# Kernel optimization log

Measured on AMD Instinct MI355X. Metric: run time of the kernel, lower is better.

Reference implementation:

```python
import jax, jax.numpy as jnp
import numpy as np

HIDDEN = 1024
SENT = 1024
NS = 8192
NK = 8192


def setup_inputs() -> dict:
    key = jax.random.key(0)
    ks = jax.random.split(key, 6)
    scale = 0.02
    return {
        "sentences_embedding": jax.random.normal(ks[0], (NS, SENT), dtype=jnp.float32),
        "knowledge_embedding": jax.random.normal(ks[1], (NK, 2 * HIDDEN), dtype=jnp.float32),
        "Ws": jax.random.normal(ks[2], (HIDDEN, SENT), dtype=jnp.float32) * scale,
        "bs": jnp.zeros((HIDDEN,), dtype=jnp.float32),
        "Wk": jax.random.normal(ks[3], (HIDDEN, 2 * HIDDEN), dtype=jnp.float32) * scale,
        "bk": jnp.zeros((HIDDEN,), dtype=jnp.float32),
    }


def reference(sentences_embedding, knowledge_embedding, Ws, bs, Wk, bk):
    # S: [Ns, hidden], K: [Nk, hidden] (torch Linear: x @ W.T + b)
    S = sentences_embedding @ Ws.T + bs
    K = knowledge_embedding @ Wk.T + bk
    V = knowledge_embedding  # [Nk, 2*hidden]
    scores = S @ K.T  # [Ns, Nk]
    # NOTE: softmax over dim=0 (across sentences), per the original module
    attns = jax.nn.softmax(scores, axis=0)
    fused_knowledge = attns @ V  # [Ns, 2*hidden]
    return (attns, fused_knowledge)
```

## Files before the change

kernel.cpp:

```cpp
#include <hip/hip_runtime.h>
#include <hip/hip_bf16.h>
#include <math.h>

typedef __bf16 bf16_t;
typedef __bf16 bf16x8 __attribute__((ext_vector_type(8)));
typedef __bf16 bf16x4v __attribute__((ext_vector_type(4)));
typedef float floatx4 __attribute__((ext_vector_type(4)));

#define BM 128
#define BN 128
#define BK 64
#define LDT 72

__device__ __forceinline__ void gload_lds16(const void* g, void* l) {
    __builtin_amdgcn_global_load_lds(
        (__attribute__((address_space(1))) void*)g,
        (__attribute__((address_space(3))) void*)l,
        16, 0, 0);
}

__device__ __forceinline__ void split8(const float* p, bf16x8& hi, bf16x8& lo) {
    const float4* q = (const float4*)p;
    float4 a = q[0], b = q[1];
    float v[8] = { a.x, a.y, a.z, a.w, b.x, b.y, b.z, b.w };
#pragma unroll
    for (int i = 0; i < 8; ++i) {
        bf16_t h = (bf16_t)v[i];
        hi[i] = h;
        lo[i] = (bf16_t)(v[i] - (float)h);
    }
}

__device__ __forceinline__ bf16x8 ld8cvt(const float* p) {
    const float4* q = (const float4*)p;
    float4 a = q[0], b = q[1];
    bf16x8 r;
    r[0] = (bf16_t)a.x; r[1] = (bf16_t)a.y; r[2] = (bf16_t)a.z; r[3] = (bf16_t)a.w;
    r[4] = (bf16_t)b.x; r[5] = (bf16_t)b.y; r[6] = (bf16_t)b.z; r[7] = (bf16_t)b.w;
    return r;
}

template<bool OUT_SPLIT, bool HAS_BIAS>
__global__ __launch_bounds__(256, 2)
void gemm_nt_split(const float* __restrict__ A, const float* __restrict__ B,
                   const float* __restrict__ bias,
                   void* __restrict__ C0, bf16_t* __restrict__ Clo,
                   int M, int N, int K)
{
    __shared__ bf16_t Ah[BM * LDT];
    __shared__ bf16_t Al[BM * LDT];
    __shared__ bf16_t Bh[BN * LDT];
    __shared__ bf16_t Bl[BN * LDT];

    const int t    = threadIdx.x;
    const int m0   = blockIdx.x * BM;
    const int n0   = blockIdx.y * BN;
    const int lane = t & 63;
    const int wm   = ((t >> 6) & 1) * 64;
    const int wn   = (t >> 7) * 64;
    const int lr   = lane & 15;
    const int lg   = lane >> 4;

    floatx4 acc[4][4] = {};

    for (int k0 = 0; k0 < K; k0 += BK) {
#pragma unroll
        for (int i = 0; i < 4; ++i) {
            int idx = t + i * 256;
            int row = idx >> 3;
            int col = (idx & 7) << 3;
            bf16x8 h, l;
            split8(&A[(size_t)(m0 + row) * K + k0 + col], h, l);
            *(bf16x8*)&Ah[row * LDT + col] = h;
            *(bf16x8*)&Al[row * LDT + col] = l;
            split8(&B[(size_t)(n0 + row) * K + k0 + col], h, l);
            *(bf16x8*)&Bh[row * LDT + col] = h;
            *(bf16x8*)&Bl[row * LDT + col] = l;
        }
        __syncthreads();
#pragma unroll
        for (int ks = 0; ks < BK; ks += 32) {
            bf16x8 ah[4], al[4], bh[4], bl[4];
#pragma unroll
            for (int mi = 0; mi < 4; ++mi) {
                ah[mi] = *(const bf16x8*)&Ah[(wm + mi * 16 + lr) * LDT + ks + lg * 8];
                al[mi] = *(const bf16x8*)&Al[(wm + mi * 16 + lr) * LDT + ks + lg * 8];
            }
#pragma unroll
            for (int ni = 0; ni < 4; ++ni) {
                bh[ni] = *(const bf16x8*)&Bh[(wn + ni * 16 + lr) * LDT + ks + lg * 8];
                bl[ni] = *(const bf16x8*)&Bl[(wn + ni * 16 + lr) * LDT + ks + lg * 8];
            }
#pragma unroll
            for (int mi = 0; mi < 4; ++mi)
#pragma unroll
                for (int ni = 0; ni < 4; ++ni) {
                    acc[mi][ni] = __builtin_amdgcn_mfma_f32_16x16x32_bf16(ah[mi], bh[ni], acc[mi][ni], 0, 0, 0);
                    acc[mi][ni] = __builtin_amdgcn_mfma_f32_16x16x32_bf16(ah[mi], bl[ni], acc[mi][ni], 0, 0, 0);
                    acc[mi][ni] = __builtin_amdgcn_mfma_f32_16x16x32_bf16(al[mi], bh[ni], acc[mi][ni], 0, 0, 0);
                }
        }
        __syncthreads();
    }

#pragma unroll
    for (int mi = 0; mi < 4; ++mi)
#pragma unroll
        for (int ni = 0; ni < 4; ++ni) {
            int col = n0 + wn + ni * 16 + lr;
            float bv = 0.0f;
            if constexpr (HAS_BIAS) bv = bias[col];
#pragma unroll
            for (int r = 0; r < 4; ++r) {
                int row = m0 + wm + mi * 16 + lg * 4 + r;
                float v = acc[mi][ni][r] + bv;
                if constexpr (OUT_SPLIT) {
                    bf16_t h = (bf16_t)v;
                    ((bf16_t*)C0)[(size_t)row * N + col] = h;
                    Clo[(size_t)row * N + col] = (bf16_t)(v - (float)h);
                } else {
                    ((float*)C0)[(size_t)row * N + col] = v;
                }
            }
        }
}

__global__ __launch_bounds__(256, 2)
void gemm_nt_pre_async(const bf16_t* __restrict__ Ahi, const bf16_t* __restrict__ Alo,
                       const bf16_t* __restrict__ Bhi, const bf16_t* __restrict__ Blo,
                       float* __restrict__ C, int M, int N, int K)
{
    __shared__ bf16_t Ah[BM * BK];
    __shared__ bf16_t Al[BM * BK];
    __shared__ bf16_t Bh[BN * BK];
    __shared__ bf16_t Bl[BN * BK];

    const int t    = threadIdx.x;
    const int m0   = blockIdx.x * BM;
    const int n0   = blockIdx.y * BN;
    const int lane = t & 63;
    const int wv   = t >> 6;
    const int wm   = ((t >> 6) & 1) * 64;
    const int wn   = (t >> 7) * 64;
    const int lr   = lane & 15;
    const int lg   = lane >> 4;
    const int lrow = lane >> 3;
    const int lcol = (((lane & 7) ^ lrow) * 8);
    const int swz  = (lr & 7) << 3;

    floatx4 acc[4][4] = {};

    for (int k0 = 0; k0 < K; k0 += BK) {
#pragma unroll
        for (int i = 0; i < 4; ++i) {
            const int seg = wv * 4 + i;
            const int row = seg * 8 + lrow;
            const size_t ga = (size_t)(m0 + row) * K + k0 + lcol;
            const size_t gb = (size_t)(n0 + row) * K + k0 + lcol;
            gload_lds16(&Ahi[ga], &Ah[seg * 512]);
            gload_lds16(&Alo[ga], &Al[seg * 512]);
            gload_lds16(&Bhi[gb], &Bh[seg * 512]);
            gload_lds16(&Blo[gb], &Bl[seg * 512]);
        }
        __syncthreads();
#pragma unroll
        for (int ks = 0; ks < BK; ks += 32) {
            const int cA = (ks + lg * 8) ^ swz;
            bf16x8 ah[4], al[4], bh[4], bl[4];
#pragma unroll
            for (int mi = 0; mi < 4; ++mi) {
                ah[mi] = *(const bf16x8*)&Ah[(wm + mi * 16 + lr) * BK + cA];
                al[mi] = *(const bf16x8*)&Al[(wm + mi * 16 + lr) * BK + cA];
            }
#pragma unroll
            for (int ni = 0; ni < 4; ++ni) {
                bh[ni] = *(const bf16x8*)&Bh[(wn + ni * 16 + lr) * BK + cA];
                bl[ni] = *(const bf16x8*)&Bl[(wn + ni * 16 + lr) * BK + cA];
            }
#pragma unroll
            for (int mi = 0; mi < 4; ++mi)
#pragma unroll
                for (int ni = 0; ni < 4; ++ni) {
                    acc[mi][ni] = __builtin_amdgcn_mfma_f32_16x16x32_bf16(ah[mi], bh[ni], acc[mi][ni], 0, 0, 0);
                    acc[mi][ni] = __builtin_amdgcn_mfma_f32_16x16x32_bf16(ah[mi], bl[ni], acc[mi][ni], 0, 0, 0);
                    acc[mi][ni] = __builtin_amdgcn_mfma_f32_16x16x32_bf16(al[mi], bh[ni], acc[mi][ni], 0, 0, 0);
                }
        }
        __syncthreads();
    }

#pragma unroll
    for (int mi = 0; mi < 4; ++mi)
#pragma unroll
        for (int ni = 0; ni < 4; ++ni) {
            int col = n0 + wn + ni * 16 + lr;
#pragma unroll
            for (int r = 0; r < 4; ++r) {
                int row = m0 + wm + mi * 16 + lg * 4 + r;
                C[(size_t)row * N + col] = acc[mi][ni][r];
            }
        }
}

__global__ __launch_bounds__(256, 2)
void gemm_nt_bf16_async(const bf16_t* __restrict__ A, const bf16_t* __restrict__ B,
                        float* __restrict__ C, int M, int N, int K)
{
    __shared__ bf16_t As[BM * BK];
    __shared__ bf16_t Bs[BN * BK];

    const int t    = threadIdx.x;
    const int m0   = blockIdx.x * BM;
    const int n0   = blockIdx.y * BN;
    const int lane = t & 63;
    const int wv   = t >> 6;
    const int wm   = ((t >> 6) & 1) * 64;
    const int wn   = (t >> 7) * 64;
    const int lr   = lane & 15;
    const int lg   = lane >> 4;
    const int lrow = lane >> 3;
    const int lcol = (((lane & 7) ^ lrow) * 8);
    const int swz  = (lr & 7) << 3;

    floatx4 acc[4][4] = {};

    for (int k0 = 0; k0 < K; k0 += BK) {
#pragma unroll
        for (int i = 0; i < 4; ++i) {
            const int seg = wv * 4 + i;
            const int row = seg * 8 + lrow;
            gload_lds16(&A[(size_t)(m0 + row) * K + k0 + lcol], &As[seg * 512]);
            gload_lds16(&B[(size_t)(n0 + row) * K + k0 + lcol], &Bs[seg * 512]);
        }
        __syncthreads();
#pragma unroll
        for (int ks = 0; ks < BK; ks += 32) {
            const int cA = (ks + lg * 8) ^ swz;
            bf16x8 a[4], b[4];
#pragma unroll
            for (int mi = 0; mi < 4; ++mi)
                a[mi] = *(const bf16x8*)&As[(wm + mi * 16 + lr) * BK + cA];
#pragma unroll
            for (int ni = 0; ni < 4; ++ni)
                b[ni] = *(const bf16x8*)&Bs[(wn + ni * 16 + lr) * BK + cA];
#pragma unroll
            for (int mi = 0; mi < 4; ++mi)
#pragma unroll
                for (int ni = 0; ni < 4; ++ni)
                    acc[mi][ni] = __builtin_amdgcn_mfma_f32_16x16x32_bf16(
                        a[mi], b[ni], acc[mi][ni], 0, 0, 0);
        }
        __syncthreads();
    }

#pragma unroll
    for (int mi = 0; mi < 4; ++mi)
#pragma unroll
        for (int ni = 0; ni < 4; ++ni) {
            int col = n0 + wn + ni * 16 + lr;
#pragma unroll
            for (int r = 0; r < 4; ++r) {
                int row = m0 + wm + mi * 16 + lg * 4 + r;
                C[(size_t)row * N + col] = acc[mi][ni][r];
            }
        }
}

__global__ __launch_bounds__(256, 2)
void gemm_nn_f32(const float* __restrict__ A, const float* __restrict__ B,
                 float* __restrict__ C, int M, int N, int K)
{
    __shared__ bf16_t As[BM * LDT];
    __shared__ bf16_t Bs[BN * LDT];

    const int t    = threadIdx.x;
    const int m0   = blockIdx.x * BM;
    const int n0   = blockIdx.y * BN;
    const int lane = t & 63;
    const int wm   = ((t >> 6) & 1) * 64;
    const int wn   = (t >> 7) * 64;
    const int lr   = lane & 15;
    const int lg   = lane >> 4;

    floatx4 acc[4][4] = {};

    for (int k0 = 0; k0 < K; k0 += BK) {
#pragma unroll
        for (int i = 0; i < 4; ++i) {
            int idx = t + i * 256;
            int row = idx >> 3;
            int col = (idx & 7) << 3;
            *(bf16x8*)&As[row * LDT + col] = ld8cvt(&A[(size_t)(m0 + row) * K + k0 + col]);
        }
#pragma unroll
        for (int i = 0; i < 2; ++i) {
            int idx = t + i * 256;
            int pn  = (idx & 31) << 2;
            int pk  = (idx >> 5) << 2;
            const float* src = &B[(size_t)(k0 + pk) * N + n0 + pn];
            float4 r0 = *(const float4*)(src);
            float4 r1 = *(const float4*)(src + N);
            float4 r2 = *(const float4*)(src + 2 * (size_t)N);
            float4 r3 = *(const float4*)(src + 3 * (size_t)N);
            bf16x4v c0 = { (bf16_t)r0.x, (bf16_t)r1.x, (bf16_t)r2.x, (bf16_t)r3.x };
            bf16x4v c1 = { (bf16_t)r0.y, (bf16_t)r1.y, (bf16_t)r2.y, (bf16_t)r3.y };
            bf16x4v c2 = { (bf16_t)r0.z, (bf16_t)r1.z, (bf16_t)r2.z, (bf16_t)r3.z };
            bf16x4v c3 = { (bf16_t)r0.w, (bf16_t)r1.w, (bf16_t)r2.w, (bf16_t)r3.w };
            *(bf16x4v*)&Bs[(pn + 0) * LDT + pk] = c0;
            *(bf16x4v*)&Bs[(pn + 1) * LDT + pk] = c1;
            *(bf16x4v*)&Bs[(pn + 2) * LDT + pk] = c2;
            *(bf16x4v*)&Bs[(pn + 3) * LDT + pk] = c3;
        }
        __syncthreads();
#pragma unroll
        for (int ks = 0; ks < BK; ks += 32) {
            bf16x8 af[4], bfr[4];
#pragma unroll
            for (int mi = 0; mi < 4; ++mi)
                af[mi] = *(const bf16x8*)&As[(wm + mi * 16 + lr) * LDT + ks + lg * 8];
#pragma unroll
            for (int ni = 0; ni < 4; ++ni)
                bfr[ni] = *(const bf16x8*)&Bs[(wn + ni * 16 + lr) * LDT + ks + lg * 8];
#pragma unroll
            for (int mi = 0; mi < 4; ++mi)
#pragma unroll
                for (int ni = 0; ni < 4; ++ni)
                    acc[mi][ni] = __builtin_amdgcn_mfma_f32_16x16x32_bf16(
                        af[mi], bfr[ni], acc[mi][ni], 0, 0, 0);
        }
        __syncthreads();
    }

#pragma unroll
    for (int mi = 0; mi < 4; ++mi)
#pragma unroll
        for (int ni = 0; ni < 4; ++ni) {
            int col = n0 + wn + ni * 16 + lr;
#pragma unroll
            for (int r = 0; r < 4; ++r) {
                int row = m0 + wm + mi * 16 + lg * 4 + r;
                C[(size_t)row * N + col] = acc[mi][ni][r];
            }
        }
}

__global__ __launch_bounds__(256)
void transpose_to_bf16(const float* __restrict__ src, bf16_t* __restrict__ dst,
                       int R, int Ccols)
{
    __shared__ float tile[64][65];
    const int r0 = blockIdx.x * 64;
    const int c0 = blockIdx.y * 64;
    const int tr = threadIdx.x >> 4;
    const int tc = (threadIdx.x & 15) * 4;
#pragma unroll
    for (int i = 0; i < 4; ++i) {
        int r = tr + i * 16;
        float4 v = *(const float4*)&src[(size_t)(r0 + r) * Ccols + c0 + tc];
        tile[r][tc + 0] = v.x; tile[r][tc + 1] = v.y;
        tile[r][tc + 2] = v.z; tile[r][tc + 3] = v.w;
    }
    __syncthreads();
#pragma unroll
    for (int i = 0; i < 4; ++i) {
        int c = tr + i * 16;
        bf16x4v o = { (bf16_t)tile[tc + 0][c], (bf16_t)tile[tc + 1][c],
                      (bf16_t)tile[tc + 2][c], (bf16_t)tile[tc + 3][c] };
        *(bf16x4v*)&dst[(size_t)(c0 + c) * R + r0 + tc] = o;
    }
}

__global__ __launch_bounds__(256)
void col_softmax_partial(const float* __restrict__ sc,
                         float* __restrict__ pm, float* __restrict__ pz)
{
    int j = blockIdx.x * 256 + threadIdx.x;
    int c = blockIdx.y;
    const float* p = sc + (size_t)c * 256 * 8192 + j;
    float m = -INFINITY, z = 0.0f;
#pragma unroll 4
    for (int i = 0; i < 256; ++i) {
        float x = p[(size_t)i * 8192];
        if (x > m) { z = z * __expf(m - x) + 1.0f; m = x; }
        else       { z += __expf(x - m); }
    }
    pm[c * 8192 + j] = m;
    pz[c * 8192 + j] = z;
}

__global__ __launch_bounds__(256)
void col_softmax_combine(const float* __restrict__ pm, const float* __restrict__ pz,
                         float* __restrict__ mf, float* __restrict__ iz)
{
    int j = blockIdx.x * 256 + threadIdx.x;
    float m = -INFINITY;
#pragma unroll
    for (int c = 0; c < 32; ++c) m = fmaxf(m, pm[c * 8192 + j]);
    float z = 0.0f;
#pragma unroll
    for (int c = 0; c < 32; ++c) z += pz[c * 8192 + j] * __expf(pm[c * 8192 + j] - m);
    mf[j] = m;
    iz[j] = 1.0f / z;
}

__global__ __launch_bounds__(256)
void normalize_attn(float* __restrict__ sc, const float* __restrict__ mf,
                    const float* __restrict__ iz)
{
    size_t base = ((size_t)blockIdx.x * 256 + threadIdx.x) * 4;
    int j = (int)(base & 8191);
    float4 s  = *(float4*)&sc[base];
    float4 m4 = *(const float4*)&mf[j];
    float4 z4 = *(const float4*)&iz[j];
    s.x = __expf(s.x - m4.x) * z4.x;
    s.y = __expf(s.y - m4.y) * z4.y;
    s.z = __expf(s.z - m4.z) * z4.z;
    s.w = __expf(s.w - m4.w) * z4.w;
    *(float4*)&sc[base] = s;
}

__global__ __launch_bounds__(256)
void normalize_attn_bf16(float* __restrict__ sc, const float* __restrict__ mf,
                         const float* __restrict__ iz, bf16_t* __restrict__ ab)
{
    size_t base = ((size_t)blockIdx.x * 256 + threadIdx.x) * 4;
    int j = (int)(base & 8191);
    float4 s  = *(float4*)&sc[base];
    float4 m4 = *(const float4*)&mf[j];
    float4 z4 = *(const float4*)&iz[j];
    s.x = __expf(s.x - m4.x) * z4.x;
    s.y = __expf(s.y - m4.y) * z4.y;
    s.z = __expf(s.z - m4.z) * z4.z;
    s.w = __expf(s.w - m4.w) * z4.w;
    *(float4*)&sc[base] = s;
    bf16x4v b = { (bf16_t)s.x, (bf16_t)s.y, (bf16_t)s.z, (bf16_t)s.w };
    *(bf16x4v*)&ab[base] = b;
}

extern "C" void kernel_launch(void* const* d_in, const int* in_sizes, int n_in,
                              void* d_out, int out_size, void* d_ws, size_t ws_size,
                              hipStream_t stream) {
    const float* sent  = (const float*)d_in[0];
    const float* knowl = (const float*)d_in[1];
    const float* Ws    = (const float*)d_in[2];
    const float* bs    = (const float*)d_in[3];
    const float* Wk    = (const float*)d_in[4];
    const float* bk    = (const float*)d_in[5];

    float* attns = (float*)d_out;
    float* fused = (float*)d_out + (size_t)8192 * 8192;

    const size_t MB = 1024 * 1024;
    char* ws = (char*)d_ws;
    bf16_t* Shi = (bf16_t*)(ws + 0 * MB);
    bf16_t* Slo = (bf16_t*)(ws + 16 * MB);
    bf16_t* Khi = (bf16_t*)(ws + 32 * MB);
    bf16_t* Klo = (bf16_t*)(ws + 48 * MB);

    dim3 blk(256);
    gemm_nt_split<true, true><<<dim3(64, 8), blk, 0, stream>>>(
        sent, Ws, bs, Shi, Slo, 8192, 1024, 1024);
    gemm_nt_split<true, true><<<dim3(64, 8), blk, 0, stream>>>(
        knowl, Wk, bk, Khi, Klo, 8192, 1024, 2048);

    const size_t NEED = 164 * MB;
    if (ws_size >= NEED) {
        bf16_t* Ab = (bf16_t*)(ws);
        bf16_t* Vt = (bf16_t*)(ws + 128 * MB);
        float*  pm = (float*)(ws + 160 * MB);
        float*  pz = pm + 32 * 8192;
        float*  mf = pz + 32 * 8192;
        float*  iz = mf + 8192;

        transpose_to_bf16<<<dim3(128, 32), blk, 0, stream>>>(knowl, Vt, 8192, 2048);
        gemm_nt_pre_async<<<dim3(64, 64), blk, 0, stream>>>(
            Shi, Slo, Khi, Klo, attns, 8192, 8192, 1024);
        col_softmax_partial<<<dim3(32, 32), blk, 0, stream>>>(attns, pm, pz);
        col_softmax_combine<<<dim3(32), blk, 0, stream>>>(pm, pz, mf, iz);
        normalize_attn_bf16<<<dim3(65536), blk, 0, stream>>>(attns, mf, iz, Ab);
        gemm_nt_bf16_async<<<dim3(64, 16), blk, 0, stream>>>(
            Ab, Vt, fused, 8192, 2048, 8192);
    } else {
        float* pm = (float*)(ws + 64 * MB);
        float* pz = pm + 32 * 8192;
        float* mf = pz + 32 * 8192;
        float* iz = mf + 8192;

        gemm_nt_pre_async<<<dim3(64, 64), blk, 0, stream>>>(
            Shi, Slo, Khi, Klo, attns, 8192, 8192, 1024);
        col_softmax_partial<<<dim3(32, 32), blk, 0, stream>>>(attns, pm, pz);
        col_softmax_combine<<<dim3(32), blk, 0, stream>>>(pm, pz, mf, iz);
        normalize_attn<<<dim3(65536), blk, 0, stream>>>(attns, mf, iz);
        gemm_nn_f32<<<dim3(64, 16), blk, 0, stream>>>(
            attns, knowl, fused, 8192, 2048, 8192);
    }
}
```

Before: 1.387 ms.

## Double-buffer LDS tiles in NT GEMM kernels to overlap loads with MFMA

Both NT GEMM kernels now keep two LDS tile buffers and prefetch the next k-tile through global_load_lds while computing on the current one, with a single barrier per iteration. The split-precision kernel also drops to a 32-wide k-tile with a new swizzle, so its LDS use stays at 64KB for the double buffer. The aim is to hide global-memory latency behind the matrix math. In exchange there are more loop iterations and barriers for the split kernel, and the non-split kernel's LDS doubles, which may limit occupancy.

```diff
diff --git a/kernel.cpp b/kernel.cpp
--- a/kernel.cpp
+++ b/kernel.cpp
@@ -130,10 +130,93 @@
                        const bf16_t* __restrict__ Bhi, const bf16_t* __restrict__ Blo,
                        float* __restrict__ C, int M, int N, int K)
 {
-    __shared__ bf16_t Ah[BM * BK];
-    __shared__ bf16_t Al[BM * BK];
-    __shared__ bf16_t Bh[BN * BK];
-    __shared__ bf16_t Bl[BN * BK];
+    __shared__ bf16_t Ah[2][BM * 32];
+    __shared__ bf16_t Al[2][BM * 32];
+    __shared__ bf16_t Bh[2][BN * 32];
+    __shared__ bf16_t Bl[2][BN * 32];
+
+    const int t    = threadIdx.x;
+    const int m0   = blockIdx.x * BM;
+    const int n0   = blockIdx.y * BN;
+    const int lane = t & 63;
+    const int wv   = t >> 6;
+    const int wm   = ((t >> 6) & 1) * 64;
+    const int wn   = (t >> 7) * 64;
+    const int lr   = lane & 15;
+    const int lg   = lane >> 4;
+
+    const int srow = lane >> 2;
+    const int scol = ((lane & 3) ^ ((lane >> 3) & 3)) << 3;
+    const int cswz = ((lg ^ ((lr >> 1) & 3)) << 3);
+
+    floatx4 acc[4][4] = {};
+
+    const int NT = K >> 5;
+
+#define STAGE_PRE(buf, kk)                                                     \
+    {                                                                          \
+        _Pragma("unroll")                                                      \
+        for (int c = 0; c < 2; ++c) {                                          \
+            const int chunk = wv * 2 + c;              \
+            const int row   = chunk * 16 + srow;                               \
+            const size_t ga = (size_t)(m0 + row) * K + (kk) + scol;            \
+            const size_t gb = (size_t)(n0 + row) * K + (kk) + scol;            \
+            gload_lds16(&Ahi[ga], &Ah[buf][chunk * 512]);                      \
+            gload_lds16(&Alo[ga], &Al[buf][chunk * 512]);                      \
+            gload_lds16(&Bhi[gb], &Bh[buf][chunk * 512]);                      \
+            gload_lds16(&Blo[gb], &Bl[buf][chunk * 512]);                      \
+        }                                                                      \
+    }
+
+    STAGE_PRE(0, 0);
+    __syncthreads();
+
+    for (int kt = 0; kt < NT; ++kt) {
+        const int cur = kt & 1;
+        if (kt + 1 < NT) STAGE_PRE(cur ^ 1, (kt + 1) << 5);
+
+        bf16x8 ah[4], al[4], bh[4], bl[4];
+#pragma unroll
+        for (int mi = 0; mi < 4; ++mi) {
+            ah[mi] = *(const bf16x8*)&Ah[cur][(wm + mi * 16 + lr) * 32 + cswz];
+            al[mi] = *(const bf16x8*)&Al[cur][(wm + mi * 16 + lr) * 32 + cswz];
+        }
+#pragma unroll
+        for (int ni = 0; ni < 4; ++ni) {
+            bh[ni] = *(const bf16x8*)&Bh[cur][(wn + ni * 16 + lr) * 32 + cswz];
+            bl[ni] = *(const bf16x8*)&Bl[cur][(wn + ni * 16 + lr) * 32 + cswz];
+        }
+#pragma unroll
+        for (int mi = 0; mi < 4; ++mi)
+#pragma unroll
+            for (int ni = 0; ni < 4; ++ni) {
+                acc[mi][ni] = __builtin_amdgcn_mfma_f32_16x16x32_bf16(ah[mi], bh[ni], acc[mi][ni], 0, 0, 0);
+                acc[mi][ni] = __builtin_amdgcn_mfma_f32_16x16x32_bf16(ah[mi], bl[ni], acc[mi][ni], 0, 0, 0);
+                acc[mi][ni] = __builtin_amdgcn_mfma_f32_16x16x32_bf16(al[mi], bh[ni], acc[mi][ni], 0, 0, 0);
+            }
+        __syncthreads();
+    }
+#undef STAGE_PRE
+
+#pragma unroll
+    for (int mi = 0; mi < 4; ++mi)
+#pragma unroll
+        for (int ni = 0; ni < 4; ++ni) {
+            int col = n0 + wn + ni * 16 + lr;
+#pragma unroll
+            for (int r = 0; r < 4; ++r) {
+                int row = m0 + wm + mi * 16 + lg * 4 + r;
+                C[(size_t)row * N + col] = acc[mi][ni][r];
+            }
+        }
+}
+
+__global__ __launch_bounds__(256, 2)
+void gemm_nt_bf16_async(const bf16_t* __restrict__ A, const bf16_t* __restrict__ B,
+                        float* __restrict__ C, int M, int N, int K)
+{
+    __shared__ bf16_t As[2][BM * BK];
+    __shared__ bf16_t Bs[2][BN * BK];
 
     const int t    = threadIdx.x;
     const int m0   = blockIdx.x * BM;
@@ -150,99 +233,38 @@
 
     floatx4 acc[4][4] = {};
 
-    for (int k0 = 0; k0 < K; k0 += BK) {
-#pragma unroll
-        for (int i = 0; i < 4; ++i) {
-            const int seg = wv * 4 + i;
-            const int row = seg * 8 + lrow;
-            const size_t ga = (size_t)(m0 + row) * K + k0 + lcol;
-            const size_t gb = (size_t)(n0 + row) * K + k0 + lcol;
-            gload_lds16(&Ahi[ga], &Ah[seg * 512]);
-            gload_lds16(&Alo[ga], &Al[seg * 512]);
-            gload_lds16(&Bhi[gb], &Bh[seg * 512]);
-            gload_lds16(&Blo[gb], &Bl[seg * 512]);
-        }
-        __syncthreads();
-#pragma unroll
-        for (int ks = 0; ks < BK; ks += 32) {
-            const int cA = (ks + lg * 8) ^ swz;
-            bf16x8 ah[4], al[4], bh[4], bl[4];
-#pragma unroll
-            for (int mi = 0; mi < 4; ++mi) {
-                ah[mi] = *(const bf16x8*)&Ah[(wm + mi * 16 + lr) * BK + cA];
-                al[mi] = *(const bf16x8*)&Al[(wm + mi * 16 + lr) * BK + cA];
-            }
-#pragma unroll
-            for (int ni = 0; ni < 4; ++ni) {
-                bh[ni] = *(const bf16x8*)&Bh[(wn + ni * 16 + lr) * BK + cA];
-                bl[ni] = *(const bf16x8*)&Bl[(wn + ni * 16 + lr) * BK + cA];
-            }
-#pragma unroll
-            for (int mi = 0; mi < 4; ++mi)
-#pragma unroll
-                for (int ni = 0; ni < 4; ++ni) {
-                    acc[mi][ni] = __builtin_amdgcn_mfma_f32_16x16x32_bf16(ah[mi], bh[ni], acc[mi][ni], 0, 0, 0);
-                    acc[mi][ni] = __builtin_amdgcn_mfma_f32_16x16x32_bf16(ah[mi], bl[ni], acc[mi][ni], 0, 0, 0);
-                    acc[mi][ni] = __builtin_amdgcn_mfma_f32_16x16x32_bf16(al[mi], bh[ni], acc[mi][ni], 0, 0, 0);
-                }
-        }
-        __syncthreads();
-    }
-
-#pragma unroll
-    for (int mi = 0; mi < 4; ++mi)
-#pragma unroll
-        for (int ni = 0; ni < 4; ++ni) {
-            int col = n0 + wn + ni * 16 + lr;
-#pragma unroll
-            for (int r = 0; r < 4; ++r) {
-                int row = m0 + wm + mi * 16 + lg * 4 + r;
-                C[(size_t)row * N + col] = acc[mi][ni][r];
-            }
-        }
-}
-
-__global__ __launch_bounds__(256, 2)
-void gemm_nt_bf16_async(const bf16_t* __restrict__ A, const bf16_t* __restrict__ B,
-                        float* __restrict__ C, int M, int N, int K)
-{
-    __shared__ bf16_t As[BM * BK];
-    __shared__ bf16_t Bs[BN * BK];
-
-    const int t    = threadIdx.x;
-    const int m0   = blockIdx.x * BM;
-    const int n0   = blockIdx.y * BN;
-    const int lane = t & 63;
-    const int wv   = t >> 6;
-    const int wm   = ((t >> 6) & 1) * 64;
-    const int wn   = (t >> 7) * 64;
-    const int lr   = lane & 15;
-    const int lg   = lane >> 4;
-    const int lrow = lane >> 3;
-    const int lcol = (((lane & 7) ^ lrow) * 8);
-    const int swz  = (lr & 7) << 3;
-
-    floatx4 acc[4][4] = {};
-
-    for (int k0 = 0; k0 < K; k0 += BK) {
-#pragma unroll
-        for (int i = 0; i < 4; ++i) {
-            const int seg = wv * 4 + i;
-            const int row = seg * 8 + lrow;
-            gload_lds16(&A[(size_t)(m0 + row) * K + k0 + lcol], &As[seg * 512]);
-            gload_lds16(&B[(size_t)(n0 + row) * K + k0 + lcol], &Bs[seg * 512]);
-        }
-        __syncthreads();
+    const int NT = K / BK;
+
+#define STAGE_NT(buf, kk)                                                      \
+    {                                                                          \
+        _Pragma("unroll")                                                      \
+        for (int i = 0; i < 4; ++i) {                                          \
+            const int seg = wv * 4 + i;                                        \
+            const int row = seg * 8 + lrow;                                    \
+            gload_lds16(&A[(size_t)(m0 + row) * K + (kk) + lcol],              \
+                        &As[buf][seg * 512]);                                  \
+            gload_lds16(&B[(size_t)(n0 + row) * K + (kk) + lcol],              \
+                        &Bs[buf][seg * 512]);                                  \
+        }                                                                      \
+    }
+
+    STAGE_NT(0, 0);
+    __syncthreads();
+
+    for (int kt = 0; kt < NT; ++kt) {
+        const int cur = kt & 1;
+        if (kt + 1 < NT) STAGE_NT(cur ^ 1, (kt + 1) * BK);
+
 #pragma unroll
         for (int ks = 0; ks < BK; ks += 32) {
             const int cA = (ks + lg * 8) ^ swz;
             bf16x8 a[4], b[4];
 #pragma unroll
             for (int mi = 0; mi < 4; ++mi)
-                a[mi] = *(const bf16x8*)&As[(wm + mi * 16 + lr) * BK + cA];
+                a[mi] = *(const bf16x8*)&As[cur][(wm + mi * 16 + lr) * BK + cA];
 #pragma unroll
             for (int ni = 0; ni < 4; ++ni)
-                b[ni] = *(const bf16x8*)&Bs[(wn + ni * 16 + lr) * BK + cA];
+                b[ni] = *(const bf16x8*)&Bs[cur][(wn + ni * 16 + lr) * BK + cA];
 #pragma unroll
             for (int mi = 0; mi < 4; ++mi)
 #pragma unroll
@@ -252,6 +274,7 @@
         }
         __syncthreads();
     }
+#undef STAGE_NT
 
 #pragma unroll
     for (int mi = 0; mi < 4; ++mi)
```

After: 1.519 ms. 9.5% more time.

## Fuse column-softmax partial max/sum into the scores GEMM epilogue

Applied to the files above, without the earlier changes.

The scores GEMM now computes, from its accumulators, a per-column running max and exp-sum over its 128-row tile. It reduces these across lanes with shuffles and across the two M-warps through shared memory, then writes them to 64 partial slots per column. This removes the separate col_softmax_partial kernel and its full strided read of the 8192x8192 fp32 score matrix. A 64-way combine kernel replaces the 32-way one. The cost is extra exp work and a block barrier in the GEMM epilogue, plus a larger workspace requirement. The fallback path is rewritten to use bf16 buffers at offsets that may exceed a smaller workspace.

```diff
diff --git a/kernel.cpp b/kernel.cpp
--- a/kernel.cpp
+++ b/kernel.cpp
@@ -128,12 +128,125 @@
 __global__ __launch_bounds__(256, 2)
 void gemm_nt_pre_async(const bf16_t* __restrict__ Ahi, const bf16_t* __restrict__ Alo,
                        const bf16_t* __restrict__ Bhi, const bf16_t* __restrict__ Blo,
-                       float* __restrict__ C, int M, int N, int K)
+                       float* __restrict__ C, float* __restrict__ pm,
+                       float* __restrict__ pz, int M, int N, int K)
 {
     __shared__ bf16_t Ah[BM * BK];
     __shared__ bf16_t Al[BM * BK];
     __shared__ bf16_t Bh[BN * BK];
     __shared__ bf16_t Bl[BN * BK];
+    __shared__ float red_m[2][128];
+    __shared__ float red_z[2][128];
+
+    const int t    = threadIdx.x;
+    const int m0   = blockIdx.x * BM;
+    const int n0   = blockIdx.y * BN;
+    const int lane = t & 63;
+    const int wv   = t >> 6;
+    const int widm = (t >> 6) & 1;
+    const int wm   = widm * 64;
+    const int wn   = (t >> 7) * 64;
+    const int lr   = lane & 15;
+    const int lg   = lane >> 4;
+    const int lrow = lane >> 3;
+    const int lcol = (((lane & 7) ^ lrow) * 8);
+    const int swz  = (lr & 7) << 3;
+
+    floatx4 acc[4][4] = {};
+
+    for (int k0 = 0; k0 < K; k0 += BK) {
+#pragma unroll
+        for (int i = 0; i < 4; ++i) {
+            const int seg = wv * 4 + i;
+            const int row = seg * 8 + lrow;
+            const size_t ga = (size_t)(m0 + row) * K + k0 + lcol;
+            const size_t gb = (size_t)(n0 + row) * K + k0 + lcol;
+            gload_lds16(&Ahi[ga], &Ah[seg * 512]);
+            gload_lds16(&Alo[ga], &Al[seg * 512]);
+            gload_lds16(&Bhi[gb], &Bh[seg * 512]);
+            gload_lds16(&Blo[gb], &Bl[seg * 512]);
+        }
+        __syncthreads();
+#pragma unroll
+        for (int ks = 0; ks < BK; ks += 32) {
+            const int cA = (ks + lg * 8) ^ swz;
+            bf16x8 ah[4], al[4], bh[4], bl[4];
+#pragma unroll
+            for (int mi = 0; mi < 4; ++mi) {
+                ah[mi] = *(const bf16x8*)&Ah[(wm + mi * 16 + lr) * BK + cA];
+                al[mi] = *(const bf16x8*)&Al[(wm + mi * 16 + lr) * BK + cA];
+            }
+#pragma unroll
+            for (int ni = 0; ni < 4; ++ni) {
+                bh[ni] = *(const bf16x8*)&Bh[(wn + ni * 16 + lr) * BK + cA];
+                bl[ni] = *(const bf16x8*)&Bl[(wn + ni * 16 + lr) * BK + cA];
+            }
+#pragma unroll
+            for (int mi = 0; mi < 4; ++mi)
+#pragma unroll
+                for (int ni = 0; ni < 4; ++ni) {
+                    acc[mi][ni] = __builtin_amdgcn_mfma_f32_16x16x32_bf16(ah[mi], bh[ni], acc[mi][ni], 0, 0, 0);
+                    acc[mi][ni] = __builtin_amdgcn_mfma_f32_16x16x32_bf16(ah[mi], bl[ni], acc[mi][ni], 0, 0, 0);
+                    acc[mi][ni] = __builtin_amdgcn_mfma_f32_16x16x32_bf16(al[mi], bh[ni], acc[mi][ni], 0, 0, 0);
+                }
+        }
+        __syncthreads();
+    }
+
+#pragma unroll
+    for (int mi = 0; mi < 4; ++mi)
+#pragma unroll
+        for (int ni = 0; ni < 4; ++ni) {
+            int col = n0 + wn + ni * 16 + lr;
+#pragma unroll
+            for (int r = 0; r < 4; ++r) {
+                int row = m0 + wm + mi * 16 + lg * 4 + r;
+                C[(size_t)row * N + col] = acc[mi][ni][r];
+            }
+        }
+
+#pragma unroll
+    for (int ni = 0; ni < 4; ++ni) {
+        float lm = -INFINITY;
+#pragma unroll
+        for (int mi = 0; mi < 4; ++mi)
+#pragma unroll
+            for (int r = 0; r < 4; ++r) lm = fmaxf(lm, acc[mi][ni][r]);
+        float lz = 0.0f;
+#pragma unroll
+        for (int mi = 0; mi < 4; ++mi)
+#pragma unroll
+            for (int r = 0; r < 4; ++r) lz += __expf(acc[mi][ni][r] - lm);
+#pragma unroll
+        for (int off = 16; off <= 32; off <<= 1) {
+            float om = __shfl_xor(lm, off);
+            float oz = __shfl_xor(lz, off);
+            float nm = fmaxf(lm, om);
+            lz = lz * __expf(lm - nm) + oz * __expf(om - nm);
+            lm = nm;
+        }
+        if (lg == 0) {
+            red_m[widm][wn + ni * 16 + lr] = lm;
+            red_z[widm][wn + ni * 16 + lr] = lz;
+        }
+    }
+    __syncthreads();
+    if (t < 128) {
+        float a = red_m[0][t], b = red_m[1][t];
+        float za = red_z[0][t], zb = red_z[1][t];
+        float mb = fmaxf(a, b);
+        float z  = za * __expf(a - mb) + zb * __expf(b - mb);
+        pm[(size_t)blockIdx.x * 8192 + n0 + t] = mb;
+        pz[(size_t)blockIdx.x * 8192 + n0 + t] = z;
+    }
+}
+
+__global__ __launch_bounds__(256, 2)
+void gemm_nt_bf16_async(const bf16_t* __restrict__ A, const bf16_t* __restrict__ B,
+                        float* __restrict__ C, int M, int N, int K)
+{
+    __shared__ bf16_t As[BM * BK];
+    __shared__ bf16_t Bs[BN * BK];
 
     const int t    = threadIdx.x;
     const int m0   = blockIdx.x * BM;
@@ -155,80 +268,6 @@
         for (int i = 0; i < 4; ++i) {
             const int seg = wv * 4 + i;
             const int row = seg * 8 + lrow;
-            const size_t ga = (size_t)(m0 + row) * K + k0 + lcol;
-            const size_t gb = (size_t)(n0 + row) * K + k0 + lcol;
-            gload_lds16(&Ahi[ga], &Ah[seg * 512]);
-            gload_lds16(&Alo[ga], &Al[seg * 512]);
-            gload_lds16(&Bhi[gb], &Bh[seg * 512]);
-            gload_lds16(&Blo[gb], &Bl[seg * 512]);
-        }
-        __syncthreads();
-#pragma unroll
-        for (int ks = 0; ks < BK; ks += 32) {
-            const int cA = (ks + lg * 8) ^ swz;
-            bf16x8 ah[4], al[4], bh[4], bl[4];
-#pragma unroll
-            for (int mi = 0; mi < 4; ++mi) {
-                ah[mi] = *(const bf16x8*)&Ah[(wm + mi * 16 + lr) * BK + cA];
-                al[mi] = *(const bf16x8*)&Al[(wm + mi * 16 + lr) * BK + cA];
-            }
-#pragma unroll
-            for (int ni = 0; ni < 4; ++ni) {
-                bh[ni] = *(const bf16x8*)&Bh[(wn + ni * 16 + lr) * BK + cA];
-                bl[ni] = *(const bf16x8*)&Bl[(wn + ni * 16 + lr) * BK + cA];
-            }
-#pragma unroll
-            for (int mi = 0; mi < 4; ++mi)
-#pragma unroll
-                for (int ni = 0; ni < 4; ++ni) {
-                    acc[mi][ni] = __builtin_amdgcn_mfma_f32_16x16x32_bf16(ah[mi], bh[ni], acc[mi][ni], 0, 0, 0);
-                    acc[mi][ni] = __builtin_amdgcn_mfma_f32_16x16x32_bf16(ah[mi], bl[ni], acc[mi][ni], 0, 0, 0);
-                    acc[mi][ni] = __builtin_amdgcn_mfma_f32_16x16x32_bf16(al[mi], bh[ni], acc[mi][ni], 0, 0, 0);
-                }
-        }
-        __syncthreads();
-    }
-
-#pragma unroll
-    for (int mi = 0; mi < 4; ++mi)
-#pragma unroll
-        for (int ni = 0; ni < 4; ++ni) {
-            int col = n0 + wn + ni * 16 + lr;
-#pragma unroll
-            for (int r = 0; r < 4; ++r) {
-                int row = m0 + wm + mi * 16 + lg * 4 + r;
-                C[(size_t)row * N + col] = acc[mi][ni][r];
-            }
-        }
-}
-
-__global__ __launch_bounds__(256, 2)
-void gemm_nt_bf16_async(const bf16_t* __restrict__ A, const bf16_t* __restrict__ B,
-                        float* __restrict__ C, int M, int N, int K)
-{
-    __shared__ bf16_t As[BM * BK];
-    __shared__ bf16_t Bs[BN * BK];
-
-    const int t    = threadIdx.x;
-    const int m0   = blockIdx.x * BM;
-    const int n0   = blockIdx.y * BN;
-    const int lane = t & 63;
-    const int wv   = t >> 6;
-    const int wm   = ((t >> 6) & 1) * 64;
-    const int wn   = (t >> 7) * 64;
-    const int lr   = lane & 15;
-    const int lg   = lane >> 4;
-    const int lrow = lane >> 3;
-    const int lcol = (((lane & 7) ^ lrow) * 8);
-    const int swz  = (lr & 7) << 3;
-
-    floatx4 acc[4][4] = {};
-
-    for (int k0 = 0; k0 < K; k0 += BK) {
-#pragma unroll
-        for (int i = 0; i < 4; ++i) {
-            const int seg = wv * 4 + i;
-            const int row = seg * 8 + lrow;
             gload_lds16(&A[(size_t)(m0 + row) * K + k0 + lcol], &As[seg * 512]);
             gload_lds16(&B[(size_t)(n0 + row) * K + k0 + lcol], &Bs[seg * 512]);
         }
@@ -249,84 +288,6 @@
                 for (int ni = 0; ni < 4; ++ni)
                     acc[mi][ni] = __builtin_amdgcn_mfma_f32_16x16x32_bf16(
                         a[mi], b[ni], acc[mi][ni], 0, 0, 0);
-        }
-        __syncthreads();
-    }
-
-#pragma unroll
-    for (int mi = 0; mi < 4; ++mi)
-#pragma unroll
-        for (int ni = 0; ni < 4; ++ni) {
-            int col = n0 + wn + ni * 16 + lr;
-#pragma unroll
-            for (int r = 0; r < 4; ++r) {
-                int row = m0 + wm + mi * 16 + lg * 4 + r;
-                C[(size_t)row * N + col] = acc[mi][ni][r];
-            }
-        }
-}
-
-__global__ __launch_bounds__(256, 2)
-void gemm_nn_f32(const float* __restrict__ A, const float* __restrict__ B,
-                 float* __restrict__ C, int M, int N, int K)
-{
-    __shared__ bf16_t As[BM * LDT];
-    __shared__ bf16_t Bs[BN * LDT];
-
-    const int t    = threadIdx.x;
-    const int m0   = blockIdx.x * BM;
-    const int n0   = blockIdx.y * BN;
-    const int lane = t & 63;
-    const int wm   = ((t >> 6) & 1) * 64;
-    const int wn   = (t >> 7) * 64;
-    const int lr   = lane & 15;
-    const int lg   = lane >> 4;
-
-    floatx4 acc[4][4] = {};
-
-    for (int k0 = 0; k0 < K; k0 += BK) {
-#pragma unroll
-        for (int i = 0; i < 4; ++i) {
-            int idx = t + i * 256;
-            int row = idx >> 3;
-            int col = (idx & 7) << 3;
-            *(bf16x8*)&As[row * LDT + col] = ld8cvt(&A[(size_t)(m0 + row) * K + k0 + col]);
-        }
-#pragma unroll
-        for (int i = 0; i < 2; ++i) {
-            int idx = t + i * 256;
-            int pn  = (idx & 31) << 2;
-            int pk  = (idx >> 5) << 2;
-            const float* src = &B[(size_t)(k0 + pk) * N + n0 + pn];
-            float4 r0 = *(const float4*)(src);
-            float4 r1 = *(const float4*)(src + N);
-            float4 r2 = *(const float4*)(src + 2 * (size_t)N);
-            float4 r3 = *(const float4*)(src + 3 * (size_t)N);
-            bf16x4v c0 = { (bf16_t)r0.x, (bf16_t)r1.x, (bf16_t)r2.x, (bf16_t)r3.x };
-            bf16x4v c1 = { (bf16_t)r0.y, (bf16_t)r1.y, (bf16_t)r2.y, (bf16_t)r3.y };
-            bf16x4v c2 = { (bf16_t)r0.z, (bf16_t)r1.z, (bf16_t)r2.z, (bf16_t)r3.z };
-            bf16x4v c3 = { (bf16_t)r0.w, (bf16_t)r1.w, (bf16_t)r2.w, (bf16_t)r3.w };
-            *(bf16x4v*)&Bs[(pn + 0) * LDT + pk] = c0;
-            *(bf16x4v*)&Bs[(pn + 1) * LDT + pk] = c1;
-            *(bf16x4v*)&Bs[(pn + 2) * LDT + pk] = c2;
-            *(bf16x4v*)&Bs[(pn + 3) * LDT + pk] = c3;
-        }
-        __syncthreads();
-#pragma unroll
-        for (int ks = 0; ks < BK; ks += 32) {
-            bf16x8 af[4], bfr[4];
-#pragma unroll
-            for (int mi = 0; mi < 4; ++mi)
-                af[mi] = *(const bf16x8*)&As[(wm + mi * 16 + lr) * LDT + ks + lg * 8];
-#pragma unroll
-            for (int ni = 0; ni < 4; ++ni)
-                bfr[ni] = *(const bf16x8*)&Bs[(wn + ni * 16 + lr) * LDT + ks + lg * 8];
-#pragma unroll
-            for (int mi = 0; mi < 4; ++mi)
-#pragma unroll
-                for (int ni = 0; ni < 4; ++ni)
-                    acc[mi][ni] = __builtin_amdgcn_mfma_f32_16x16x32_bf16(
-                        af[mi], bfr[ni], acc[mi][ni], 0, 0, 0);
         }
         __syncthreads();
     }
@@ -371,34 +332,16 @@
 }
 
 __global__ __launch_bounds__(256)
-void col_softmax_partial(const float* __restrict__ sc,
-                         float* __restrict__ pm, float* __restrict__ pz)
-{
-    int j = blockIdx.x * 256 + threadIdx.x;
-    int c = blockIdx.y;
-    const float* p = sc + (size_t)c * 256 * 8192 + j;
-    float m = -INFINITY, z = 0.0f;
-#pragma unroll 4
-    for (int i = 0; i < 256; ++i) {
-        float x = p[(size_t)i * 8192];
-        if (x > m) { z = z * __expf(m - x) + 1.0f; m = x; }
-        else       { z += __expf(x - m); }
-    }
-    pm[c * 8192 + j] = m;
-    pz[c * 8192 + j] = z;
-}
-
-__global__ __launch_bounds__(256)
-void col_softmax_combine(const float* __restrict__ pm, const float* __restrict__ pz,
-                         float* __restrict__ mf, float* __restrict__ iz)
+void col_softmax_combine64(const float* __restrict__ pm, const float* __restrict__ pz,
+                           float* __restrict__ mf, float* __restrict__ iz)
 {
     int j = blockIdx.x * 256 + threadIdx.x;
     float m = -INFINITY;
 #pragma unroll
-    for (int c = 0; c < 32; ++c) m = fmaxf(m, pm[c * 8192 + j]);
+    for (int c = 0; c < 64; ++c) m = fmaxf(m, pm[(size_t)c * 8192 + j]);
     float z = 0.0f;
 #pragma unroll
-    for (int c = 0; c < 32; ++c) z += pz[c * 8192 + j] * __expf(pm[c * 8192 + j] - m);
+    for (int c = 0; c < 64; ++c) z += pz[(size_t)c * 8192 + j] * __expf(pm[(size_t)c * 8192 + j] - m);
     mf[j] = m;
     iz[j] = 1.0f / z;
 }
@@ -463,35 +406,36 @@
     gemm_nt_split<true, true><<<dim3(64, 8), blk, 0, stream>>>(
         knowl, Wk, bk, Khi, Klo, 8192, 1024, 2048);
 
-    const size_t NEED = 164 * MB;
+    const size_t NEED = 166 * MB;
     if (ws_size >= NEED) {
         bf16_t* Ab = (bf16_t*)(ws);
         bf16_t* Vt = (bf16_t*)(ws + 128 * MB);
         float*  pm = (float*)(ws + 160 * MB);
-        float*  pz = pm + 32 * 8192;
-        float*  mf = pz + 32 * 8192;
+        float*  pz = (float*)(ws + 162 * MB);
+        float*  mf = (float*)(ws + 164 * MB);
         float*  iz = mf + 8192;
 
         transpose_to_bf16<<<dim3(128, 32), blk, 0, stream>>>(knowl, Vt, 8192, 2048);
         gemm_nt_pre_async<<<dim3(64, 64), blk, 0, stream>>>(
-            Shi, Slo, Khi, Klo, attns, 8192, 8192, 1024);
-        col_softmax_partial<<<dim3(32, 32), blk, 0, stream>>>(attns, pm, pz);
-        col_softmax_combine<<<dim3(32), blk, 0, stream>>>(pm, pz, mf, iz);
+            Shi, Slo, Khi, Klo, attns, pm, pz, 8192, 8192, 1024);
+        col_softmax_combine64<<<dim3(32), blk, 0, stream>>>(pm, pz, mf, iz);
         normalize_attn_bf16<<<dim3(65536), blk, 0, stream>>>(attns, mf, iz, Ab);
         gemm_nt_bf16_async<<<dim3(64, 16), blk, 0, stream>>>(
             Ab, Vt, fused, 8192, 2048, 8192);
     } else {
         float* pm = (float*)(ws + 64 * MB);
-        float* pz = pm + 32 * 8192;
-        float* mf = pz + 32 * 8192;
+        float* pz = (float*)(ws + 66 * MB);
+        float* mf = (float*)(ws + 68 * MB);
         float* iz = mf + 8192;
 
         gemm_nt_pre_async<<<dim3(64, 64), blk, 0, stream>>>(
-            Shi, Slo, Khi, Klo, attns, 8192, 8192, 1024);
-        col_softmax_partial<<<dim3(32, 32), blk, 0, stream>>>(attns, pm, pz);
-        col_softmax_combine<<<dim3(32), blk, 0, stream>>>(pm, pz, mf, iz);
-        normalize_attn<<<dim3(65536), blk, 0, stream>>>(attns, mf, iz);
-        gemm_nn_f32<<<dim3(64, 16), blk, 0, stream>>>(
-            attns, knowl, fused, 8192, 2048, 8192);
-    }
-}
+            Shi, Slo, Khi, Klo, attns, pm, pz, 8192, 8192, 1024);
+        col_softmax_combine64<<<dim3(32), blk, 0, stream>>>(pm, pz, mf, iz);
+        bf16_t* Ab = (bf16_t*)(ws);
+        normalize_attn_bf16<<<dim3(65536), blk, 0, stream>>>(attns, mf, iz, Ab);
+        bf16_t* Vt = (bf16_t*)(ws + 128 * MB);
+        transpose_to_bf16<<<dim3(128, 32), blk, 0, stream>>>(knowl, Vt, 8192, 2048);
+        gemm_nt_bf16_async<<<dim3(64, 16), blk, 0, stream>>>(
+            Ab, Vt, fused, 8192, 2048, 8192);
+    }
+}
```

Result: faster. 1.286 ms (-7.3%).
